# Optimization experiments

Hardware: AMD Instinct MI355X
Metric: run time of the kernel (lower is better)

The kernel has to match this reference:

```python
import jax, jax.numpy as jnp
import numpy as np

B, C, H, W = 2, 192, 64, 64
HEADS, KS = 6, 7
HD = C // HEADS


def setup_inputs() -> dict:
    key = jax.random.key(0)
    ks = jax.random.split(key, 6)
    s = 0.02
    return {
        "x": jax.random.normal(ks[0], (B, C, H, W), jnp.float32),
        "W_qkv1": jax.random.normal(ks[1], (3 * C, C, 1, 1), jnp.float32) * s,
        "b_qkv1": jnp.zeros((3 * C,), jnp.float32),
        "W_qkv2": jax.random.normal(ks[2], (3 * C, 1, 3, 3), jnp.float32) * s,  # depthwise
        "b_qkv2": jnp.zeros((3 * C,), jnp.float32),
        "temperature": jnp.ones((HEADS, 1, 1, 1), jnp.float32),
        "rpb": jax.random.normal(ks[3], (HEADS, 2 * KS - 1, 2 * KS - 1), jnp.float32) * s,
        "W_proj": jax.random.normal(ks[4], (C, C, 1, 1), jnp.float32) * s,
        "b_proj": jnp.zeros((C,), jnp.float32),
    }


def _conv(x, w, b, pad, groups=1):
    y = jax.lax.conv_general_dilated(
        x, w, (1, 1), pad,
        dimension_numbers=("NCHW", "OIHW", "NCHW"),
        feature_group_count=groups)
    return y + b[None, :, None, None]


def _l2norm(t, eps=1e-12):
    n = jnp.sqrt(jnp.sum(t * t, axis=-1, keepdims=True))
    return t / jnp.maximum(n, eps)


def _nbr_idx(L, K):
    # NATTEN shifted-window neighborhood (dilation=1): window start clamped to image.
    start = jnp.clip(jnp.arange(L) - K // 2, 0, L - K)
    idx = start[:, None] + jnp.arange(K)[None, :]        # [L,K] absolute neighbor index
    rel = idx - jnp.arange(L)[:, None] + (K - 1)         # [L,K] rpb table index
    return idx, rel


def _forward(x, W_qkv1, b_qkv1, W_qkv2, b_qkv2, temperature, rpb, W_proj, b_proj):
    Bq, Cq, Hh, Ww = x.shape
    heads = rpb.shape[0]
    K = (rpb.shape[1] + 1) // 2
    hd = Cq // heads
    qkv = _conv(_conv(x, W_qkv1, b_qkv1, "VALID"), W_qkv2, b_qkv2, "SAME", groups=3 * Cq)
    qkv = qkv.reshape(Bq, 3, heads, hd, Hh, Ww).transpose(1, 0, 2, 4, 5, 3)  # [3,B,h,H,W,d]
    q, k, v = qkv[0], qkv[1], qkv[2]
    q = _l2norm(q)
    k = _l2norm(k)
    idx_i, rel_i = _nbr_idx(Hh, K)
    idx_j, rel_j = _nbr_idx(Ww, K)
    ii = idx_i[:, None, :, None]  # [H,1,K,1]
    jj = idx_j[None, :, None, :]  # [1,W,1,K] -> broadcast [H,W,K,K]
    k_nb = k[:, :, ii, jj, :]     # [B,h,H,W,K,K,d]
    attn = jnp.einsum("bhijd,bhijkld->bhijkl", q, k_nb)
    bias = rpb[:, rel_i[:, None, :, None], rel_j[None, :, None, :]]  # [h,H,W,K,K]
    attn = (attn + bias[None]) * temperature.reshape(1, heads, 1, 1, 1, 1)
    attn = jax.nn.softmax(attn.reshape(Bq, heads, Hh, Ww, K * K), axis=-1)
    v_nb = v[:, :, ii, jj, :].reshape(Bq, heads, Hh, Ww, K * K, hd)
    out = jnp.einsum("bhijk,bhijkd->bhijd", attn, v_nb)
    out = out.transpose(0, 1, 4, 2, 3).reshape(Bq, Cq, Hh, Ww)
    return _conv(out, W_proj, b_proj, "VALID")


def reference(x, W_qkv1, b_qkv1, W_qkv2, b_qkv2, temperature, rpb, W_proj, b_proj):
    return _forward(x, W_qkv1, b_qkv1, W_qkv2, b_qkv2, temperature, rpb, W_proj, b_proj)
```

## Files before the change

kernel.cpp:

```cpp
#include <hip/hip_runtime.h>
#include <math.h>

#define HW 4096

typedef __attribute__((ext_vector_type(8))) short short8;
typedef __attribute__((ext_vector_type(8))) _Float16 half8;
typedef __attribute__((ext_vector_type(4))) float floatx4;

__device__ inline float bflo(unsigned u) { return __uint_as_float(u << 16); }
__device__ inline float bfhi(unsigned u) { return __uint_as_float(u & 0xffff0000u); }
__device__ inline unsigned short f2bf(float x) {
    unsigned u = __float_as_uint(x);
    return (unsigned short)((u + 0x7fffu + ((u >> 16) & 1u)) >> 16);
}
__device__ inline unsigned f2bf2(float lo, float hi) {
    unsigned a = __float_as_uint(lo), b = __float_as_uint(hi);
    a = (a + 0x7fffu + ((a >> 16) & 1u)) >> 16;
    b = (b + 0x7fffu + ((b >> 16) & 1u)) & 0xffff0000u;
    return a | b;
}
__device__ inline unsigned short f2h(float x) {
    _Float16 h = (_Float16)x;
    return __builtin_bit_cast(unsigned short, h);
}


__global__ __launch_bounds__(256) void k_cvt(const float* __restrict__ W1,
    const float* __restrict__ Wp, unsigned short* __restrict__ Wb1,
    unsigned short* __restrict__ Wbp)
{
    int idx = blockIdx.x * 256 + threadIdx.x;
    if (idx < 110592) Wb1[idx] = f2bf(W1[idx]);
    else if (idx < 147456) Wbp[idx - 110592] = f2bf(Wp[idx - 110592]);
}

__global__ __launch_bounds__(256) void k_xt(const float* __restrict__ x,
    unsigned short* __restrict__ xT)
{
    __shared__ float smf[64 * 65];
    const int t = threadIdx.x;
    const int px0 = blockIdx.x << 6;
    const int c0 = blockIdx.y << 6;
    const int b = blockIdx.z;
    const float* xb = x + ((size_t)(b * 192 + c0) << 12) + px0;
    const int pxl = t & 63, csub = t >> 6;
    #pragma unroll
    for (int pass = 0; pass < 16; ++pass) {
        int c = pass * 4 + csub;
        smf[pxl * 65 + c] = xb[((size_t)c << 12) + pxl];
    }
    __syncthreads();
    const int c2 = t & 31, psub = t >> 5;
    unsigned* ob = (unsigned*)xT;
    #pragma unroll
    for (int pass = 0; pass < 8; ++pass) {
        int px = pass * 8 + psub;
        unsigned v = f2bf2(smf[px * 65 + c2 * 2], smf[px * 65 + c2 * 2 + 1]);
        ob[((size_t)((b << 12) + px0 + px)) * 96 + (c0 >> 1) + c2] = v;
    }
}

__global__ __launch_bounds__(256) void k_gq(const unsigned short* __restrict__ xT,
    const unsigned short* __restrict__ Wb1, const float* __restrict__ b1,
    unsigned short* __restrict__ qkv)
{
    __shared__ __align__(16) unsigned short As[64 * 200];
    __shared__ __align__(16) unsigned short Bs[64 * 200];
    const int t = threadIdx.x;
    const int m0 = blockIdx.x * 64;
    const int n0 = blockIdx.y * 64;
    #pragma unroll
    for (int pass = 0; pass < 6; ++pass) {
        int idx = pass * 256 + t;
        int m = idx / 24, c16 = idx % 24;
        *(uint4*)&As[m * 200 + c16 * 8] = *(const uint4*)&xT[(size_t)(m0 + m) * 192 + c16 * 8];
        *(uint4*)&Bs[m * 200 + c16 * 8] = *(const uint4*)&Wb1[(size_t)(n0 + m) * 192 + c16 * 8];
    }
    __syncthreads();
    const int w = t >> 6, lane = t & 63;
    const int lm = lane & 15, lq = lane >> 4;
    floatx4 acc[4] = {};
    #pragma unroll
    for (int ks = 0; ks < 6; ++ks) {
        short8 bf = *(const short8*)&Bs[(w * 16 + lm) * 200 + ks * 32 + lq * 8];
        #pragma unroll
        for (int mt = 0; mt < 4; ++mt) {
            short8 af = *(const short8*)&As[(mt * 16 + lm) * 200 + ks * 32 + lq * 8];
            acc[mt] = __builtin_amdgcn_mfma_f32_16x16x32_bf16(af, bf, acc[mt], 0, 0, 0);
        }
    }
    __syncthreads();
    const float bias = b1[n0 + w * 16 + lm];
    #pragma unroll
    for (int mt = 0; mt < 4; ++mt)
        #pragma unroll
        for (int r = 0; r < 4; ++r)
            As[(mt * 16 + lq * 4 + r) * 72 + w * 16 + lm] = f2bf(acc[mt][r] + bias);
    __syncthreads();
    #pragma unroll
    for (int pass = 0; pass < 2; ++pass) {
        int idx = pass * 256 + t;
        int m = idx >> 3, n8 = idx & 7;
        uint4 val = *(const uint4*)&As[m * 72 + n8 * 8];
        int mg = m0 + m;
        int b = mg >> 12, px = mg & 4095;
        int oc = n0 + n8 * 8;
        int g = oc >> 5, d = oc & 31;
        *(uint4*)&qkv[((((size_t)(b * 18 + g) << 12) + px) << 5) + d] = val;
    }
}

__global__ __launch_bounds__(256) void k_dw(const unsigned short* __restrict__ in,
    const float* __restrict__ W2, const float* __restrict__ b2,
    unsigned short* __restrict__ outq)
{
    __shared__ float wsm[288];
    __shared__ float bsm[32];
    const int t = threadIdx.x;
    const int bg = blockIdx.y;
    const int g = (bg >= 18) ? bg - 18 : bg;
    const int cbase = (g / 6) * 192 + (g % 6) * 32;
    for (int idx = t; idx < 288; idx += 256)
        wsm[idx] = W2[(cbase + (idx & 31)) * 9 + (idx >> 5)];
    if (t < 32) bsm[t] = b2[cbase + t];
    __syncthreads();
    const int px = (blockIdx.x << 6) + (t >> 2);
    const int d8 = t & 3;
    const int i = px >> 6, j = px & 63;
    const unsigned short* base = in + ((size_t)bg << 17);
    float acc[8];
    #pragma unroll
    for (int e = 0; e < 8; ++e) acc[e] = bsm[d8 * 8 + e];
    #pragma unroll
    for (int di = -1; di <= 1; ++di) {
        int ii = i + di;
        if (ii < 0 || ii > 63) continue;
        #pragma unroll
        for (int dj = -1; dj <= 1; ++dj) {
            int jj = j + dj;
            if (jj < 0 || jj > 63) continue;
            int tap = (di + 1) * 3 + dj + 1;
            uint4 u = *(const uint4*)(base + ((((ii << 6) + jj) << 5) + d8 * 8));
            const float* wt = &wsm[tap * 32 + d8 * 8];
            acc[0] = fmaf(bflo(u.x), wt[0], acc[0]);
            acc[1] = fmaf(bfhi(u.x), wt[1], acc[1]);
            acc[2] = fmaf(bflo(u.y), wt[2], acc[2]);
            acc[3] = fmaf(bfhi(u.y), wt[3], acc[3]);
            acc[4] = fmaf(bflo(u.z), wt[4], acc[4]);
            acc[5] = fmaf(bfhi(u.z), wt[5], acc[5]);
            acc[6] = fmaf(bflo(u.w), wt[6], acc[6]);
            acc[7] = fmaf(bfhi(u.w), wt[7], acc[7]);
        }
    }
    uint4 o;
    o.x = f2bf2(acc[0], acc[1]); o.y = f2bf2(acc[2], acc[3]);
    o.z = f2bf2(acc[4], acc[5]); o.w = f2bf2(acc[6], acc[7]);
    *(uint4*)(outq + ((size_t)bg << 17) + ((size_t)px << 5) + d8 * 8) = o;
}

__global__ __launch_bounds__(256) void k_attn(const unsigned short* __restrict__ qkv,
    const float* __restrict__ temp, const float* __restrict__ rpb,
    unsigned short* __restrict__ attnO)
{
    __shared__ __align__(16) char lds[45224];
    unsigned short* Ks  = (unsigned short*)lds;
    unsigned short* Ps  = (unsigned short*)lds;
    unsigned short* Vts = (unsigned short*)(lds + 29696);
    float* rpbs = (float*)(lds + 44544);

    const int t = threadIdx.x;
    const int ti = blockIdx.x >> 3, tj = blockIdx.x & 7;
    const int head = blockIdx.y, b = blockIdx.z;
    const int i0 = ti * 8, j0 = tj * 8;
    const int r0 = min(max(i0 - 3, 0), 50), c0 = min(max(j0 - 3, 0), 50);
    const unsigned short* qpl = qkv + ((size_t)(b * 18 + head) << 17);
    const unsigned short* kpl = qkv + ((size_t)(b * 18 + 6 + head) << 17);
    const unsigned short* vpl = qkv + ((size_t)(b * 18 + 12 + head) << 17);

    if (t < 196) {
        int r = (t * 2341) >> 15, cc = t - r * 14;
        int pix = ((r0 + r) << 6) + (c0 + cc);
        const uint4* kg = (const uint4*)(kpl + (pix << 5));
        const uint4* vg = (const uint4*)(vpl + (pix << 5));
        float kf[32];
        float ss = 0.f;
        #pragma unroll
        for (int q = 0; q < 4; ++q) {
            uint4 ku = kg[q];
            unsigned uu[4] = {ku.x, ku.y, ku.z, ku.w};
            #pragma unroll
            for (int e = 0; e < 4; ++e) {
                float lo = bflo(uu[e]), hi = bfhi(uu[e]);
                kf[q * 8 + e * 2] = lo; kf[q * 8 + e * 2 + 1] = hi;
                ss = fmaf(lo, lo, fmaf(hi, hi, ss));
            }
        }
        float rinv = 1.0f / fmaxf(sqrtf(ss), 1e-12f);
        #pragma unroll
        for (int q = 0; q < 4; ++q) {
            uint4 p;
            p.x = f2bf2(kf[q * 8 + 0] * rinv, kf[q * 8 + 1] * rinv);
            p.y = f2bf2(kf[q * 8 + 2] * rinv, kf[q * 8 + 3] * rinv);
            p.z = f2bf2(kf[q * 8 + 4] * rinv, kf[q * 8 + 5] * rinv);
            p.w = f2bf2(kf[q * 8 + 6] * rinv, kf[q * 8 + 7] * rinv);
            *(uint4*)&Ks[t * 40 + q * 8] = p;
        }
        #pragma unroll
        for (int q = 0; q < 4; ++q) {
            uint4 vu = vg[q];
            unsigned uu[4] = {vu.x, vu.y, vu.z, vu.w};
            #pragma unroll
            for (int e = 0; e < 4; ++e) {
                Vts[(q * 8 + e * 2) * 232 + t]     = f2h(bflo(uu[e]));
                Vts[(q * 8 + e * 2 + 1) * 232 + t] = f2h(bfhi(uu[e]));
            }
        }
    }
    for (int idx = t; idx < 448; idx += 256) {
        int row = (idx * 2341) >> 15;
        int c = idx - row * 14;
        ((unsigned*)(Vts + row * 232))[98 + c] = 0u;
    }
    if (t < 169) rpbs[t] = rpb[head * 169 + t];

    const int w = t >> 6, lane = t & 63;
    const int lm = lane & 15, lq = lane >> 4;
    const int px = w * 16 + lm;
    const int i = i0 + (px >> 3), j = j0 + (px & 7);
    uint4 qu = *(const uint4*)(qpl + ((((i << 6) + j) << 5) + lq * 8));
    float qf[8];
    qf[0] = bflo(qu.x); qf[1] = bfhi(qu.x);
    qf[2] = bflo(qu.y); qf[3] = bfhi(qu.y);
    qf[4] = bflo(qu.z); qf[5] = bfhi(qu.z);
    qf[6] = bflo(qu.w); qf[7] = bfhi(qu.w);
    float qs = 0.f;
    #pragma unroll
    for (int e = 0; e < 8; ++e) qs = fmaf(qf[e], qf[e], qs);
    qs += __shfl_xor(qs, 16);
    qs += __shfl_xor(qs, 32);
    float qinv = 1.0f / fmaxf(sqrtf(qs), 1e-12f);
    short8 bq;
    #pragma unroll
    for (int e = 0; e < 8; ++e) bq[e] = (short)f2bf(qf[e] * qinv);
    __syncthreads();

    floatx4 acc[13];
    #pragma unroll
    for (int mt = 0; mt < 13; ++mt) {
        short8 ak = *(const short8*)&Ks[(mt * 16 + lm) * 40 + lq * 8];
        floatx4 z = {0.f, 0.f, 0.f, 0.f};
        acc[mt] = __builtin_amdgcn_mfma_f32_16x16x32_bf16(ak, bq, z, 0, 0, 0);
    }
    __syncthreads();

    const int si = min(max(i - 3, 0), 57), sj = min(max(j - 3, 0), 57);
    const int vloi = si - r0, vloj = sj - c0;
    const int oi = r0 - i + 6, oj = c0 - j + 6;
    const float th = temp[head];
    float mx = -1e30f;
    #pragma unroll
    for (int mt = 0; mt < 13; ++mt) {
        int nb0 = mt * 16 + lq * 4;
        int rh0 = (nb0 * 2341) >> 15;
        int ch0 = nb0 - rh0 * 14;
        #pragma unroll
        for (int r = 0; r < 4; ++r) {
            int ch = ch0 + r, rh = rh0;
            if (ch >= 14) { ch -= 14; rh += 1; }
            int bidx = (rh + oi) * 13 + (ch + oj);
            float bias = rpbs[max(0, min(168, bidx))];
            bool valid = ((unsigned)(rh - vloi) <= 6u) && ((unsigned)(ch - vloj) <= 6u);
            float s = (acc[mt][r] + bias) * th;
            s = valid ? s : -1e30f;
            acc[mt][r] = s;
            mx = fmaxf(mx, s);
        }
    }
    mx = fmaxf(mx, __shfl_xor(mx, 16));
    mx = fmaxf(mx, __shfl_xor(mx, 32));
    float ssum = 0.f;
    #pragma unroll
    for (int mt = 0; mt < 13; ++mt)
        #pragma unroll
        for (int r = 0; r < 4; ++r) {
            float e = __expf(acc[mt][r] - mx);
            acc[mt][r] = e;
            ssum += e;
        }
    ssum += __shfl_xor(ssum, 16);
    ssum += __shfl_xor(ssum, 32);
    const float rs = 1.0f / ssum;

    if (lane < 32) {
        uint4 z4 = {0u, 0u, 0u, 0u};
        *(uint4*)&Ps[(w * 16 + (lane >> 1)) * 232 + 208 + (lane & 1) * 8] = z4;
    }
    #pragma unroll
    for (int mt = 0; mt < 13; ++mt) {
        unsigned lo = (unsigned)f2h(acc[mt][0] * rs) | ((unsigned)f2h(acc[mt][1] * rs) << 16);
        unsigned hi = (unsigned)f2h(acc[mt][2] * rs) | ((unsigned)f2h(acc[mt][3] * rs) << 16);
        *(uint2*)&Ps[px * 232 + mt * 16 + lq * 4] = make_uint2(lo, hi);
    }
    __syncthreads();

    floatx4 oacc[2] = {};
    #pragma unroll
    for (int ks = 0; ks < 7; ++ks) {
        half8 ap = *(const half8*)&Ps[(w * 16 + lm) * 232 + ks * 32 + lq * 8];
        #pragma unroll
        for (int n2 = 0; n2 < 2; ++n2) {
            half8 bv = *(const half8*)&Vts[(n2 * 16 + lm) * 232 + ks * 32 + lq * 8];
            oacc[n2] = __builtin_amdgcn_mfma_f32_16x16x32_f16(ap, bv, oacc[n2], 0, 0, 0);
        }
    }
    #pragma unroll
    for (int n2 = 0; n2 < 2; ++n2)
        #pragma unroll
        for (int r = 0; r < 4; ++r) {
            int p2 = w * 16 + lq * 4 + r;
            int i2 = i0 + (p2 >> 3), j2 = j0 + (p2 & 7);
            attnO[((size_t)((b << 12) + (i2 << 6) + j2)) * 192 + head * 32 + n2 * 16 + lm]
                = f2bf(oacc[n2][r]);
        }
}

__global__ __launch_bounds__(256) void k_gp(const unsigned short* __restrict__ Ain,
    const unsigned short* __restrict__ Wbp, const float* __restrict__ bp,
    float* __restrict__ out)
{
    __shared__ __align__(16) unsigned short As[64 * 200];
    __shared__ __align__(16) unsigned short Bs[64 * 200];
    const int t = threadIdx.x;
    const int m0 = blockIdx.x * 64;
    const int n0 = blockIdx.y * 64;
    #pragma unroll
    for (int pass = 0; pass < 6; ++pass) {
        int idx = pass * 256 + t;
        int m = idx / 24, c16 = idx % 24;
        *(uint4*)&As[m * 200 + c16 * 8] = *(const uint4*)&Ain[(size_t)(m0 + m) * 192 + c16 * 8];
        *(uint4*)&Bs[m * 200 + c16 * 8] = *(const uint4*)&Wbp[(size_t)(n0 + m) * 192 + c16 * 8];
    }
    __syncthreads();
    const int w = t >> 6, lane = t & 63;
    const int lm = lane & 15, lq = lane >> 4;
    floatx4 acc[4] = {};
    #pragma unroll
    for (int ks = 0; ks < 6; ++ks) {
        short8 bf = *(const short8*)&Bs[(w * 16 + lm) * 200 + ks * 32 + lq * 8];
        #pragma unroll
        for (int mt = 0; mt < 4; ++mt) {
            short8 af = *(const short8*)&As[(mt * 16 + lm) * 200 + ks * 32 + lq * 8];
            acc[mt] = __builtin_amdgcn_mfma_f32_16x16x32_bf16(af, bf, acc[mt], 0, 0, 0);
        }
    }
    __syncthreads();
    float* fs = (float*)As;
    const float bias = bp[n0 + w * 16 + lm];
    #pragma unroll
    for (int mt = 0; mt < 4; ++mt)
        #pragma unroll
        for (int r = 0; r < 4; ++r)
            fs[(w * 16 + lm) * 68 + mt * 16 + lq * 4 + r] = acc[mt][r] + bias;
    __syncthreads();
    const int b = m0 >> 12, px0 = m0 & 4095;
    #pragma unroll
    for (int pass = 0; pass < 4; ++pass) {
        int idx = pass * 256 + t;
        int n = idx >> 4, m4 = idx & 15;
        float4 val = *(const float4*)&fs[n * 68 + m4 * 4];
        *(float4*)&out[((size_t)(b * 192 + n0 + n) << 12) + px0 + m4 * 4] = val;
    }
}

extern "C" void kernel_launch(void* const* d_in, const int* in_sizes, int n_in,
                              void* d_out, int out_size, void* d_ws, size_t ws_size,
                              hipStream_t stream) {
    const float* x    = (const float*)d_in[0];
    const float* W1   = (const float*)d_in[1];
    const float* b1   = (const float*)d_in[2];
    const float* W2   = (const float*)d_in[3];
    const float* b2   = (const float*)d_in[4];
    const float* temp = (const float*)d_in[5];
    const float* rpb  = (const float*)d_in[6];
    const float* Wp   = (const float*)d_in[7];
    const float* bp   = (const float*)d_in[8];
    float* out = (float*)d_out;

    char* ws = (char*)d_ws;
    unsigned short* Wb1   = (unsigned short*)(ws);
    unsigned short* Wbp   = (unsigned short*)(ws + 221184);
    unsigned short* xT    = (unsigned short*)(ws + 294912);
    unsigned short* qkv1b = (unsigned short*)(ws + 3440640);
    unsigned short* qkv2b = (unsigned short*)(ws + 12877824);
    unsigned short* attnO = (unsigned short*)(ws + 22315008);

    k_cvt <<<dim3(576), 256, 0, stream>>>(W1, Wp, Wb1, Wbp);
    k_xt  <<<dim3(64, 3, 2), 256, 0, stream>>>(x, xT);
    k_gq  <<<dim3(128, 9), 256, 0, stream>>>(xT, Wb1, b1, qkv1b);
    k_dw  <<<dim3(64, 36), 256, 0, stream>>>(qkv1b, W2, b2, qkv2b);
    k_attn<<<dim3(64, 6, 2), 256, 0, stream>>>(qkv2b, temp, rpb, attnO);
    k_gp  <<<dim3(128, 3), 256, 0, stream>>>(attnO, Wbp, bp, out);
}
```

Measured before the change: 114.8 us.

## Fuse depthwise 3x3 conv into attention kernel and merge prep kernels

The depthwise 3x3 convolution is computed inside the attention kernel: K and V are convolved on the fly for the 14x14 halo tile from the pointwise-conv output, and Q is convolved per pixel before normalization. This removes a separate kernel launch and the write and re-read of the full post-depthwise qkv tensor. The weight conversion and x transpose kernels are also merged into one launch. In exchange, the halo tiles are convolved redundantly across neighboring blocks (9 taps each), which adds global loads and ALU work to the attention kernel and raises its LDS use.

Result: slower. 142.2 us (+23.9%).

```diff
diff --git a/kernel.cpp b/kernel.cpp
--- a/kernel.cpp
+++ b/kernel.cpp
@@ -25,23 +25,24 @@
 }
 
 
-__global__ __launch_bounds__(256) void k_cvt(const float* __restrict__ W1,
-    const float* __restrict__ Wp, unsigned short* __restrict__ Wb1,
+__global__ __launch_bounds__(256) void k_prep(const float* __restrict__ x,
+    const float* __restrict__ W1, const float* __restrict__ Wp,
+    unsigned short* __restrict__ xT, unsigned short* __restrict__ Wb1,
     unsigned short* __restrict__ Wbp)
 {
-    int idx = blockIdx.x * 256 + threadIdx.x;
-    if (idx < 110592) Wb1[idx] = f2bf(W1[idx]);
-    else if (idx < 147456) Wbp[idx - 110592] = f2bf(Wp[idx - 110592]);
-}
-
-__global__ __launch_bounds__(256) void k_xt(const float* __restrict__ x,
-    unsigned short* __restrict__ xT)
-{
+    const int t = threadIdx.x;
+    const int bx = blockIdx.x;
+    if (bx >= 384) {
+        int idx = (bx - 384) * 256 + t;
+        if (idx < 110592) Wb1[idx] = f2bf(W1[idx]);
+        else Wbp[idx - 110592] = f2bf(Wp[idx - 110592]);
+        return;
+    }
     __shared__ float smf[64 * 65];
-    const int t = threadIdx.x;
-    const int px0 = blockIdx.x << 6;
-    const int c0 = blockIdx.y << 6;
-    const int b = blockIdx.z;
+    const int px0 = (bx & 63) << 6;
+    const int rest = bx >> 6;
+    const int c0 = (rest % 3) << 6;
+    const int b = rest / 3;
     const float* xb = x + ((size_t)(b * 192 + c0) << 12) + px0;
     const int pxl = t & 63, csub = t >> 6;
     #pragma unroll
@@ -110,63 +111,18 @@
     }
 }
 
-__global__ __launch_bounds__(256) void k_dw(const unsigned short* __restrict__ in,
+__global__ __launch_bounds__(256) void k_attn(const unsigned short* __restrict__ qkv,
     const float* __restrict__ W2, const float* __restrict__ b2,
-    unsigned short* __restrict__ outq)
-{
-    __shared__ float wsm[288];
-    __shared__ float bsm[32];
-    const int t = threadIdx.x;
-    const int bg = blockIdx.y;
-    const int g = (bg >= 18) ? bg - 18 : bg;
-    const int cbase = (g / 6) * 192 + (g % 6) * 32;
-    for (int idx = t; idx < 288; idx += 256)
-        wsm[idx] = W2[(cbase + (idx & 31)) * 9 + (idx >> 5)];
-    if (t < 32) bsm[t] = b2[cbase + t];
-    __syncthreads();
-    const int px = (blockIdx.x << 6) + (t >> 2);
-    const int d8 = t & 3;
-    const int i = px >> 6, j = px & 63;
-    const unsigned short* base = in + ((size_t)bg << 17);
-    float acc[8];
-    #pragma unroll
-    for (int e = 0; e < 8; ++e) acc[e] = bsm[d8 * 8 + e];
-    #pragma unroll
-    for (int di = -1; di <= 1; ++di) {
-        int ii = i + di;
-        if (ii < 0 || ii > 63) continue;
-        #pragma unroll
-        for (int dj = -1; dj <= 1; ++dj) {
-            int jj = j + dj;
-            if (jj < 0 || jj > 63) continue;
-            int tap = (di + 1) * 3 + dj + 1;
-            uint4 u = *(const uint4*)(base + ((((ii << 6) + jj) << 5) + d8 * 8));
-            const float* wt = &wsm[tap * 32 + d8 * 8];
-            acc[0] = fmaf(bflo(u.x), wt[0], acc[0]);
-            acc[1] = fmaf(bfhi(u.x), wt[1], acc[1]);
-            acc[2] = fmaf(bflo(u.y), wt[2], acc[2]);
-            acc[3] = fmaf(bfhi(u.y), wt[3], acc[3]);
-            acc[4] = fmaf(bflo(u.z), wt[4], acc[4]);
-            acc[5] = fmaf(bfhi(u.z), wt[5], acc[5]);
-            acc[6] = fmaf(bflo(u.w), wt[6], acc[6]);
-            acc[7] = fmaf(bfhi(u.w), wt[7], acc[7]);
-        }
-    }
-    uint4 o;
-    o.x = f2bf2(acc[0], acc[1]); o.y = f2bf2(acc[2], acc[3]);
-    o.z = f2bf2(acc[4], acc[5]); o.w = f2bf2(acc[6], acc[7]);
-    *(uint4*)(outq + ((size_t)bg << 17) + ((size_t)px << 5) + d8 * 8) = o;
-}
-
-__global__ __launch_bounds__(256) void k_attn(const unsigned short* __restrict__ qkv,
     const float* __restrict__ temp, const float* __restrict__ rpb,
     unsigned short* __restrict__ attnO)
 {
-    __shared__ __align__(16) char lds[45224];
+    __shared__ __align__(16) char lds[49060];
     unsigned short* Ks  = (unsigned short*)lds;
     unsigned short* Ps  = (unsigned short*)lds;
     unsigned short* Vts = (unsigned short*)(lds + 29696);
-    float* rpbs = (float*)(lds + 44544);
+    float* wsm  = (float*)(lds + 44544);
+    float* bsm  = (float*)(lds + 48000);
+    float* rpbs = (float*)(lds + 48384);
 
     const int t = threadIdx.x;
     const int ti = blockIdx.x >> 3, tj = blockIdx.x & 7;
@@ -177,42 +133,71 @@
     const unsigned short* kpl = qkv + ((size_t)(b * 18 + 6 + head) << 17);
     const unsigned short* vpl = qkv + ((size_t)(b * 18 + 12 + head) << 17);
 
-    if (t < 196) {
-        int r = (t * 2341) >> 15, cc = t - r * 14;
-        int pix = ((r0 + r) << 6) + (c0 + cc);
-        const uint4* kg = (const uint4*)(kpl + (pix << 5));
-        const uint4* vg = (const uint4*)(vpl + (pix << 5));
-        float kf[32];
-        float ss = 0.f;
-        #pragma unroll
-        for (int q = 0; q < 4; ++q) {
-            uint4 ku = kg[q];
-            unsigned uu[4] = {ku.x, ku.y, ku.z, ku.w};
-            #pragma unroll
-            for (int e = 0; e < 4; ++e) {
-                float lo = bflo(uu[e]), hi = bfhi(uu[e]);
-                kf[q * 8 + e * 2] = lo; kf[q * 8 + e * 2 + 1] = hi;
-                ss = fmaf(lo, lo, fmaf(hi, hi, ss));
+    for (int idx = t; idx < 864; idx += 256) {
+        int pl = idx / 288, rem = idx - pl * 288;
+        int tap = rem >> 5, ch = rem & 31;
+        wsm[idx] = W2[(pl * 192 + head * 32 + ch) * 9 + tap];
+    }
+    for (int idx = t; idx < 96; idx += 256)
+        bsm[idx] = b2[(idx >> 5) * 192 + head * 32 + (idx & 31)];
+    if (t < 169) rpbs[t] = rpb[head * 169 + t];
+    __syncthreads();
+
+    const int d4 = t & 7, slot = t >> 3;
+    {
+        float4 wk4[9], wv4[9];
+        #pragma unroll
+        for (int tap = 0; tap < 9; ++tap) {
+            wk4[tap] = *(const float4*)&wsm[288 + tap * 32 + d4 * 4];
+            wv4[tap] = *(const float4*)&wsm[576 + tap * 32 + d4 * 4];
+        }
+        const float4 bk4 = *(const float4*)&bsm[32 + d4 * 4];
+        const float4 bv4 = *(const float4*)&bsm[64 + d4 * 4];
+        #pragma unroll
+        for (int ph = 0; ph < 7; ++ph) {
+            int p = slot + ph * 32;
+            bool act = p < 196;
+            float4 sk = bk4, sv = bv4;
+            if (act) {
+                int r = (p * 2341) >> 15, cc = p - r * 14;
+                int gi = r0 + r, gj = c0 + cc;
+                #pragma unroll
+                for (int di = -1; di <= 1; ++di) {
+                    int ii = gi + di;
+                    if (ii < 0 || ii > 63) continue;
+                    #pragma unroll
+                    for (int dj = -1; dj <= 1; ++dj) {
+                        int jj = gj + dj;
+                        if (jj < 0 || jj > 63) continue;
+                        int tap = (di + 1) * 3 + dj + 1;
+                        size_t off = ((size_t)((ii << 6) + jj) << 5) + d4 * 4;
+                        uint2 ku = *(const uint2*)(kpl + off);
+                        uint2 vu = *(const uint2*)(vpl + off);
+                        sk.x = fmaf(bflo(ku.x), wk4[tap].x, sk.x);
+                        sk.y = fmaf(bfhi(ku.x), wk4[tap].y, sk.y);
+                        sk.z = fmaf(bflo(ku.y), wk4[tap].z, sk.z);
+                        sk.w = fmaf(bfhi(ku.y), wk4[tap].w, sk.w);
+                        sv.x = fmaf(bflo(vu.x), wv4[tap].x, sv.x);
+                        sv.y = fmaf(bfhi(vu.x), wv4[tap].y, sv.y);
+                        sv.z = fmaf(bflo(vu.y), wv4[tap].z, sv.z);
+                        sv.w = fmaf(bfhi(vu.y), wv4[tap].w, sv.w);
+                    }
+                }
             }
-        }
-        float rinv = 1.0f / fmaxf(sqrtf(ss), 1e-12f);
-        #pragma unroll
-        for (int q = 0; q < 4; ++q) {
-            uint4 p;
-            p.x = f2bf2(kf[q * 8 + 0] * rinv, kf[q * 8 + 1] * rinv);
-            p.y = f2bf2(kf[q * 8 + 2] * rinv, kf[q * 8 + 3] * rinv);
-            p.z = f2bf2(kf[q * 8 + 4] * rinv, kf[q * 8 + 5] * rinv);
-            p.w = f2bf2(kf[q * 8 + 6] * rinv, kf[q * 8 + 7] * rinv);
-            *(uint4*)&Ks[t * 40 + q * 8] = p;
-        }
-        #pragma unroll
-        for (int q = 0; q < 4; ++q) {
-            uint4 vu = vg[q];
-            unsigned uu[4] = {vu.x, vu.y, vu.z, vu.w};
-            #pragma unroll
-            for (int e = 0; e < 4; ++e) {
-                Vts[(q * 8 + e * 2) * 232 + t]     = f2h(bflo(uu[e]));
-                Vts[(q * 8 + e * 2 + 1) * 232 + t] = f2h(bfhi(uu[e]));
+            float ss = act ? (sk.x*sk.x + sk.y*sk.y + sk.z*sk.z + sk.w*sk.w) : 0.f;
+            ss += __shfl_xor(ss, 1);
+            ss += __shfl_xor(ss, 2);
+            ss += __shfl_xor(ss, 4);
+            if (act) {
+                float rinv = 1.0f / fmaxf(sqrtf(ss), 1e-12f);
+                uint2 pk;
+                pk.x = f2bf2(sk.x * rinv, sk.y * rinv);
+                pk.y = f2bf2(sk.z * rinv, sk.w * rinv);
+                *(uint2*)&Ks[p * 40 + d4 * 4] = pk;
+                Vts[(d4 * 4 + 0) * 232 + p] = f2h(sv.x);
+                Vts[(d4 * 4 + 1) * 232 + p] = f2h(sv.y);
+                Vts[(d4 * 4 + 2) * 232 + p] = f2h(sv.z);
+                Vts[(d4 * 4 + 3) * 232 + p] = f2h(sv.w);
             }
         }
     }
@@ -221,18 +206,37 @@
         int c = idx - row * 14;
         ((unsigned*)(Vts + row * 232))[98 + c] = 0u;
     }
-    if (t < 169) rpbs[t] = rpb[head * 169 + t];
 
     const int w = t >> 6, lane = t & 63;
     const int lm = lane & 15, lq = lane >> 4;
     const int px = w * 16 + lm;
     const int i = i0 + (px >> 3), j = j0 + (px & 7);
-    uint4 qu = *(const uint4*)(qpl + ((((i << 6) + j) << 5) + lq * 8));
     float qf[8];
-    qf[0] = bflo(qu.x); qf[1] = bfhi(qu.x);
-    qf[2] = bflo(qu.y); qf[3] = bfhi(qu.y);
-    qf[4] = bflo(qu.z); qf[5] = bfhi(qu.z);
-    qf[6] = bflo(qu.w); qf[7] = bfhi(qu.w);
+    #pragma unroll
+    for (int e = 0; e < 8; ++e) qf[e] = bsm[lq * 8 + e];
+    #pragma unroll
+    for (int di = -1; di <= 1; ++di) {
+        int ii = i + di;
+        if (ii < 0 || ii > 63) continue;
+        #pragma unroll
+        for (int dj = -1; dj <= 1; ++dj) {
+            int jj = j + dj;
+            if (jj < 0 || jj > 63) continue;
+            int tap = (di + 1) * 3 + dj + 1;
+            size_t off = ((size_t)((ii << 6) + jj) << 5) + lq * 8;
+            uint4 xu = *(const uint4*)(qpl + off);
+            float4 wa = *(const float4*)&wsm[tap * 32 + lq * 8];
+            float4 wb = *(const float4*)&wsm[tap * 32 + lq * 8 + 4];
+            qf[0] = fmaf(bflo(xu.x), wa.x, qf[0]);
+            qf[1] = fmaf(bfhi(xu.x), wa.y, qf[1]);
+            qf[2] = fmaf(bflo(xu.y), wa.z, qf[2]);
+            qf[3] = fmaf(bfhi(xu.y), wa.w, qf[3]);
+            qf[4] = fmaf(bflo(xu.z), wb.x, qf[4]);
+            qf[5] = fmaf(bfhi(xu.z), wb.y, qf[5]);
+            qf[6] = fmaf(bflo(xu.w), wb.z, qf[6]);
+            qf[7] = fmaf(bfhi(xu.w), wb.w, qf[7]);
+        }
+    }
     float qs = 0.f;
     #pragma unroll
     for (int e = 0; e < 8; ++e) qs = fmaf(qf[e], qf[e], qs);
@@ -391,13 +395,10 @@
     unsigned short* Wbp   = (unsigned short*)(ws + 221184);
     unsigned short* xT    = (unsigned short*)(ws + 294912);
     unsigned short* qkv1b = (unsigned short*)(ws + 3440640);
-    unsigned short* qkv2b = (unsigned short*)(ws + 12877824);
-    unsigned short* attnO = (unsigned short*)(ws + 22315008);
-
-    k_cvt <<<dim3(576), 256, 0, stream>>>(W1, Wp, Wb1, Wbp);
-    k_xt  <<<dim3(64, 3, 2), 256, 0, stream>>>(x, xT);
+    unsigned short* attnO = (unsigned short*)(ws + 12877824);
+
+    k_prep<<<dim3(960), 256, 0, stream>>>(x, W1, Wp, xT, Wb1, Wbp);
     k_gq  <<<dim3(128, 9), 256, 0, stream>>>(xT, Wb1, b1, qkv1b);
-    k_dw  <<<dim3(64, 36), 256, 0, stream>>>(qkv1b, W2, b2, qkv2b);
-    k_attn<<<dim3(64, 6, 2), 256, 0, stream>>>(qkv2b, temp, rpb, attnO);
+    k_attn<<<dim3(64, 6, 2), 256, 0, stream>>>(qkv1b, W2, b2, temp, rpb, attnO);
     k_gp  <<<dim3(128, 3), 256, 0, stream>>>(attnO, Wbp, bp, out);
 }
```

## Fuse weight conversion and input transpose into the GEMM kernels

Applied to the files above, without the earlier changes.

Removes the separate fp32-to-bf16 weight conversion kernel and the input transpose kernel. The QKV GEMM now reads fp32 NCHW input directly, converting and transposing into shared memory, and both GEMMs convert fp32 weights to bf16 while staging them. This saves two launches and a workspace round-trip. In exchange, weights are reconverted by every block, and the strided input loads per channel may be less efficient.

Result: no change. 113.2 us (-1.4%).

```diff
diff --git a/kernel.cpp b/kernel.cpp
--- a/kernel.cpp
+++ b/kernel.cpp
@@ -25,43 +25,8 @@
 }
 
 
-__global__ __launch_bounds__(256) void k_cvt(const float* __restrict__ W1,
-    const float* __restrict__ Wp, unsigned short* __restrict__ Wb1,
-    unsigned short* __restrict__ Wbp)
-{
-    int idx = blockIdx.x * 256 + threadIdx.x;
-    if (idx < 110592) Wb1[idx] = f2bf(W1[idx]);
-    else if (idx < 147456) Wbp[idx - 110592] = f2bf(Wp[idx - 110592]);
-}
-
-__global__ __launch_bounds__(256) void k_xt(const float* __restrict__ x,
-    unsigned short* __restrict__ xT)
-{
-    __shared__ float smf[64 * 65];
-    const int t = threadIdx.x;
-    const int px0 = blockIdx.x << 6;
-    const int c0 = blockIdx.y << 6;
-    const int b = blockIdx.z;
-    const float* xb = x + ((size_t)(b * 192 + c0) << 12) + px0;
-    const int pxl = t & 63, csub = t >> 6;
-    #pragma unroll
-    for (int pass = 0; pass < 16; ++pass) {
-        int c = pass * 4 + csub;
-        smf[pxl * 65 + c] = xb[((size_t)c << 12) + pxl];
-    }
-    __syncthreads();
-    const int c2 = t & 31, psub = t >> 5;
-    unsigned* ob = (unsigned*)xT;
-    #pragma unroll
-    for (int pass = 0; pass < 8; ++pass) {
-        int px = pass * 8 + psub;
-        unsigned v = f2bf2(smf[px * 65 + c2 * 2], smf[px * 65 + c2 * 2 + 1]);
-        ob[((size_t)((b << 12) + px0 + px)) * 96 + (c0 >> 1) + c2] = v;
-    }
-}
-
-__global__ __launch_bounds__(256) void k_gq(const unsigned short* __restrict__ xT,
-    const unsigned short* __restrict__ Wb1, const float* __restrict__ b1,
+__global__ __launch_bounds__(256) void k_gq(const float* __restrict__ x,
+    const float* __restrict__ W1, const float* __restrict__ b1,
     unsigned short* __restrict__ qkv)
 {
     __shared__ __align__(16) unsigned short As[64 * 200];
@@ -69,15 +34,30 @@
     const int t = threadIdx.x;
     const int m0 = blockIdx.x * 64;
     const int n0 = blockIdx.y * 64;
-    #pragma unroll
-    for (int pass = 0; pass < 6; ++pass) {
-        int idx = pass * 256 + t;
-        int m = idx / 24, c16 = idx % 24;
-        *(uint4*)&As[m * 200 + c16 * 8] = *(const uint4*)&xT[(size_t)(m0 + m) * 192 + c16 * 8];
-        *(uint4*)&Bs[m * 200 + c16 * 8] = *(const uint4*)&Wb1[(size_t)(n0 + m) * 192 + c16 * 8];
-    }
-    __syncthreads();
     const int w = t >> 6, lane = t & 63;
+    const int b = m0 >> 12, px0 = m0 & 4095;
+    {
+        const float* xb = x + ((size_t)(b * 192) << 12) + px0 + lane;
+        const int cb = w * 48;
+        #pragma unroll
+        for (int r4 = 0; r4 < 12; ++r4) {
+            float v0 = xb[(size_t)(cb + r4 * 4 + 0) << 12];
+            float v1 = xb[(size_t)(cb + r4 * 4 + 1) << 12];
+            float v2 = xb[(size_t)(cb + r4 * 4 + 2) << 12];
+            float v3 = xb[(size_t)(cb + r4 * 4 + 3) << 12];
+            *(uint2*)&As[lane * 200 + cb + r4 * 4] =
+                make_uint2(f2bf2(v0, v1), f2bf2(v2, v3));
+        }
+    }
+    #pragma unroll
+    for (int pass = 0; pass < 12; ++pass) {
+        int idx = pass * 256 + t;
+        int row = idx / 48, ch = idx - row * 48;
+        float4 wv = *(const float4*)&W1[(size_t)(n0 + row) * 192 + ch * 4];
+        *(uint2*)&Bs[row * 200 + ch * 4] =
+            make_uint2(f2bf2(wv.x, wv.y), f2bf2(wv.z, wv.w));
+    }
+    __syncthreads();
     const int lm = lane & 15, lq = lane >> 4;
     floatx4 acc[4] = {};
     #pragma unroll
@@ -102,11 +82,9 @@
         int idx = pass * 256 + t;
         int m = idx >> 3, n8 = idx & 7;
         uint4 val = *(const uint4*)&As[m * 72 + n8 * 8];
-        int mg = m0 + m;
-        int b = mg >> 12, px = mg & 4095;
         int oc = n0 + n8 * 8;
         int g = oc >> 5, d = oc & 31;
-        *(uint4*)&qkv[((((size_t)(b * 18 + g) << 12) + px) << 5) + d] = val;
+        *(uint4*)&qkv[((((size_t)(b * 18 + g) << 12) + px0 + m) << 5) + d] = val;
     }
 }
 
@@ -325,7 +303,7 @@
 }
 
 __global__ __launch_bounds__(256) void k_gp(const unsigned short* __restrict__ Ain,
-    const unsigned short* __restrict__ Wbp, const float* __restrict__ bp,
+    const float* __restrict__ Wp, const float* __restrict__ bp,
     float* __restrict__ out)
 {
     __shared__ __align__(16) unsigned short As[64 * 200];
@@ -338,7 +316,14 @@
         int idx = pass * 256 + t;
         int m = idx / 24, c16 = idx % 24;
         *(uint4*)&As[m * 200 + c16 * 8] = *(const uint4*)&Ain[(size_t)(m0 + m) * 192 + c16 * 8];
-        *(uint4*)&Bs[m * 200 + c16 * 8] = *(const uint4*)&Wbp[(size_t)(n0 + m) * 192 + c16 * 8];
+    }
+    #pragma unroll
+    for (int pass = 0; pass < 12; ++pass) {
+        int idx = pass * 256 + t;
+        int row = idx / 48, ch = idx - row * 48;
+        float4 wv = *(const float4*)&Wp[(size_t)(n0 + row) * 192 + ch * 4];
+        *(uint2*)&Bs[row * 200 + ch * 4] =
+            make_uint2(f2bf2(wv.x, wv.y), f2bf2(wv.z, wv.w));
     }
     __syncthreads();
     const int w = t >> 6, lane = t & 63;
@@ -387,17 +372,12 @@
     float* out = (float*)d_out;
 
     char* ws = (char*)d_ws;
-    unsigned short* Wb1   = (unsigned short*)(ws);
-    unsigned short* Wbp   = (unsigned short*)(ws + 221184);
-    unsigned short* xT    = (unsigned short*)(ws + 294912);
-    unsigned short* qkv1b = (unsigned short*)(ws + 3440640);
-    unsigned short* qkv2b = (unsigned short*)(ws + 12877824);
-    unsigned short* attnO = (unsigned short*)(ws + 22315008);
-
-    k_cvt <<<dim3(576), 256, 0, stream>>>(W1, Wp, Wb1, Wbp);
-    k_xt  <<<dim3(64, 3, 2), 256, 0, stream>>>(x, xT);
-    k_gq  <<<dim3(128, 9), 256, 0, stream>>>(xT, Wb1, b1, qkv1b);
+    unsigned short* qkv1b = (unsigned short*)(ws);
+    unsigned short* qkv2b = (unsigned short*)(ws + 9437184);
+    unsigned short* attnO = (unsigned short*)(ws + 18874368);
+
+    k_gq  <<<dim3(128, 9), 256, 0, stream>>>(x, W1, b1, qkv1b);
     k_dw  <<<dim3(64, 36), 256, 0, stream>>>(qkv1b, W2, b2, qkv2b);
     k_attn<<<dim3(64, 6, 2), 256, 0, stream>>>(qkv2b, temp, rpb, attnO);
-    k_gp  <<<dim3(128, 3), 256, 0, stream>>>(attnO, Wbp, bp, out);
-}
+    k_gp  <<<dim3(128, 3), 256, 0, stream>>>(attnO, Wp, bp, out);
+}
```
